# Performance work log

Measured on AMD Instinct MI355X. Metric: run time of the kernel, lower is better.

Reference implementation:

```python
import jax, jax.numpy as jnp
import numpy as np


def _rpad(x):
    # reflect-pad by 1 on both sides along the last dim (matches torch helper)
    return jnp.concatenate([x[..., 1:2], x, x[..., -2:-1]], axis=-1)


def _fwd1d(x):
    # LeGall 5/3 forward lifting along the last dim
    even = x[..., 0::2]
    odd = x[..., 1::2]
    e = _rpad(even)
    pred = 0.5 * (e[..., :-2] + e[..., 2:])
    d = odd - pred                      # detail
    de = _rpad(d)
    upd = 0.25 * (de[..., :-2] + de[..., 2:])
    s = even + upd                      # approx
    return s, d


def setup_inputs() -> dict:
    key = jax.random.key(0)
    # (B, C, H, W) with even H, W so the odd-size reflect pad branch is inactive
    x = jax.random.normal(key, (8, 3, 1024, 1024), dtype=jnp.float32)
    return {"x": x}


def reference(x):
    # rows: transform along W (last dim)
    s_row, d_row = _fwd1d(x)
    # columns: transform along H by swapping H<->W, lifting, swapping back
    LL, LH = _fwd1d(jnp.swapaxes(s_row, 2, 3))
    HL, HH = _fwd1d(jnp.swapaxes(d_row, 2, 3))
    LL, LH, HL, HH = (jnp.swapaxes(t, 2, 3) for t in (LL, LH, HL, HH))
    # (B, 4C, H/2, W/2) subband order [LL, LH, HL, HH]
    return jnp.concatenate([LL, LH, HL, HH], axis=1)
```

## Files before the change

### kernel.cpp

```cpp
#include <hip/hip_runtime.h>


static __device__ __forceinline__ int mref(int k) {
    if (k < 0) return 1;
    if (k > 511) return 510;
    return k;
}

__global__ __launch_bounds__(256) void ilwt53_fused(const float* __restrict__ x,
                                                    float* __restrict__ out) {
    const int tid = threadIdx.x;
    const int c0  = blockIdx.x * 32;
    const int r0  = blockIdx.y * 32;
    const int img = blockIdx.z;

    const int cb = 2 * c0 - 4;
    const int rb = 2 * r0 - 4;

    __shared__ float xt[72 * 73];
    __shared__ float db[72 * 35];
    __shared__ float sb[72 * 33];

    const float* __restrict__ xim = x + (size_t)img * (1024 * 1024);

    #pragma unroll
    for (int n = 0; n < 21; ++n) {
        int i = tid + n * 256;
        if (i < 72 * 72) {
            int lr = i / 72, lc = i - lr * 72;
            int gy = rb + lr; gy = gy < 0 ? 0 : (gy > 1023 ? 1023 : gy);
            int gx = cb + lc; gx = gx < 0 ? 0 : (gx > 1023 ? 1023 : gx);
            xt[lr * 73 + lc] = xim[(size_t)gy * 1024 + gx];
        }
    }
    __syncthreads();

    for (int n = 0; n < 10; ++n) {
        int i = tid + n * 256;
        if (i < 72 * 34) {
            int lr = i / 34, j = i - lr * 34;
            int c = c0 - 1 + j;
            int km1 = mref(c - 1), kp1 = mref(c + 1);
            const float* row = xt + lr * 73;
            float o  = row[2 * (c - c0) + 5];
            float em = row[2 * (km1 - c0) + 4];
            float ep = row[2 * (kp1 - c0) + 4];
            db[lr * 35 + j] = o - 0.5f * (em + ep);
        }
    }
    __syncthreads();

    #pragma unroll
    for (int n = 0; n < 9; ++n) {
        int i = tid + n * 256;
        int lr = i / 32, jj = i & 31;
        int c = c0 + jj;
        int km1 = mref(c - 1), kp1 = mref(c + 1);
        float e  = xt[lr * 73 + 2 * jj + 4];
        float dm = db[lr * 35 + (km1 - c0 + 1)];
        float dp = db[lr * 35 + (kp1 - c0 + 1)];
        sb[lr * 33 + jj] = e + 0.25f * (dm + dp);
    }
    __syncthreads();

    const size_t plane = 512 * 512;
    float* __restrict__ ob = out + ((size_t)(img / 3) * 12 + (img % 3)) * plane;

    #pragma unroll
    for (int p = 0; p < 4; ++p) {
        int i  = tid + p * 256;
        int rr = i >> 5, cc = i & 31;
        int r = r0 + rr, c = c0 + cc;

        const float* sc = sb + cc;
        const float* dc = db + cc + 1;

        auto SE = [&](int k) { return sc[(2 * (k - r0) + 4) * 33]; };
        auto SO = [&](int k) { return sc[(2 * (k - r0) + 5) * 33]; };
        auto DE = [&](int k) { return dc[(2 * (k - r0) + 4) * 35]; };
        auto DO = [&](int k) { return dc[(2 * (k - r0) + 5) * 35]; };

        auto LHf = [&](int k) { return SO(k) - 0.5f * (SE(mref(k - 1)) + SE(mref(k + 1))); };
        auto HHf = [&](int k) { return DO(k) - 0.5f * (DE(mref(k - 1)) + DE(mref(k + 1))); };

        int km = mref(r - 1), kp = mref(r + 1);

        float lh = LHf(r);
        float ll = SE(r) + 0.25f * (LHf(km) + LHf(kp));
        float hh = HHf(r);
        float hl = DE(r) + 0.25f * (HHf(km) + HHf(kp));

        size_t o = (size_t)r * 512 + c;
        ob[o]             = ll;
        ob[o + 3 * plane] = lh;
        ob[o + 6 * plane] = hl;
        ob[o + 9 * plane] = hh;
    }
}

extern "C" void kernel_launch(void* const* d_in, const int* in_sizes, int n_in,
                              void* d_out, int out_size, void* d_ws, size_t ws_size,
                              hipStream_t stream) {
    const float* x = (const float*)d_in[0];
    float* out = (float*)d_out;
    dim3 grid(16, 16, 24);
    dim3 block(256);
    hipLaunchKernelGGL(ilwt53_fused, grid, block, 0, stream, x, out);
}
```

Baseline: 193.3 us.

## Replace shared-memory tiled kernel with register-streaming row-sliding float4 kernel

Replaces the shared-memory tile approach with a kernel where each thread owns four output columns and walks down sixteen output rows. It computes the horizontal lifting from direct float4 global row loads and keeps a sliding window of vertical lifting state in registers. This removes the LDS staging, the three block barriers and the 72x72 halo tile, and it writes outputs as float4. The cost is redundant horizontal recomputation for the halo rows at each 16-row chunk start, more registers per thread, and only 768 blocks of 128 threads.

```diff
diff --git a/kernel.cpp b/kernel.cpp
--- a/kernel.cpp
+++ b/kernel.cpp
@@ -2,99 +2,114 @@
 
 
 static __device__ __forceinline__ int mref(int k) {
-    if (k < 0) return 1;
-    if (k > 511) return 510;
-    return k;
+    return k < 0 ? 1 : (k > 511 ? 510 : k);
 }
 
-__global__ __launch_bounds__(256) void ilwt53_fused(const float* __restrict__ x,
-                                                    float* __restrict__ out) {
-    const int tid = threadIdx.x;
-    const int c0  = blockIdx.x * 32;
-    const int r0  = blockIdx.y * 32;
-    const int img = blockIdx.z;
+static __device__ __forceinline__ float4 f4_sub_half(float4 o, float4 a, float4 b) {
+    return make_float4(o.x - 0.5f * (a.x + b.x), o.y - 0.5f * (a.y + b.y),
+                       o.z - 0.5f * (a.z + b.z), o.w - 0.5f * (a.w + b.w));
+}
+static __device__ __forceinline__ float4 f4_add_q(float4 e, float4 a, float4 b) {
+    return make_float4(e.x + 0.25f * (a.x + b.x), e.y + 0.25f * (a.y + b.y),
+                       e.z + 0.25f * (a.z + b.z), e.w + 0.25f * (a.w + b.w));
+}
 
-    const int cb = 2 * c0 - 4;
-    const int rb = 2 * r0 - 4;
+struct SD { float4 s, d; };
 
-    __shared__ float xt[72 * 73];
-    __shared__ float db[72 * 35];
-    __shared__ float sb[72 * 33];
+static __device__ __forceinline__ SD hrow(const float* __restrict__ xim, int y, int fb) {
+    y = y < 0 ? 0 : (y > 1023 ? 1023 : y);
+    const float* __restrict__ row = xim + (size_t)y * 1024;
+    int fbc = fb < 0 ? 0 : (fb > 1008 ? 1008 : fb);
+
+    float w[16];
+    {
+        const float4* p = (const float4*)(row + fbc);
+        float4 v0 = p[0], v1 = p[1], v2 = p[2], v3 = p[3];
+        w[0]=v0.x; w[1]=v0.y; w[2]=v0.z; w[3]=v0.w;
+        w[4]=v1.x; w[5]=v1.y; w[6]=v1.z; w[7]=v1.w;
+        w[8]=v2.x; w[9]=v2.y; w[10]=v2.z; w[11]=v2.w;
+        w[12]=v3.x; w[13]=v3.y; w[14]=v3.z; w[15]=v3.w;
+    }
+    if (fb < 0) {
+        #pragma unroll
+        for (int q = 15; q >= 4; --q) w[q] = w[q - 4];
+    }
+    if (fb > 1008) {
+        #pragma unroll
+        for (int q = 0; q <= 11; ++q) w[q] = w[q + 4];
+    }
+
+    float d[6];
+    #pragma unroll
+    for (int t = 0; t < 6; ++t)
+        d[t] = w[2*t + 3] - 0.5f * (w[2*t] + w[2*t + 4]);
+    if (fb < 0)    d[1] = w[5]  - w[6];
+    if (fb > 1008) d[4] = w[11] - w[8];
+
+    float4 s;
+    s.x = w[4]  + 0.25f * (d[0] + d[2]);
+    s.y = w[6]  + 0.25f * (d[1] + d[3]);
+    s.z = w[8]  + 0.25f * (d[2] + d[4]);
+    s.w = w[10] + 0.25f * (d[3] + d[5]);
+    if (fb < 0)    s.x = w[4]  + 0.5f * d[2];
+    if (fb > 1008) s.w = w[10] + 0.5f * d[3];
+
+    SD r; r.s = s; r.d = make_float4(d[1], d[2], d[3], d[4]);
+    return r;
+}
+
+__global__ __launch_bounds__(128) void ilwt53_v4(const float* __restrict__ x,
+                                                 float* __restrict__ out) {
+    const int c   = 4 * threadIdx.x;
+    const int fb  = 2 * c - 4;
+    const int R   = 16 * blockIdx.x;
+    const int img = blockIdx.y;
 
     const float* __restrict__ xim = x + (size_t)img * (1024 * 1024);
+    const size_t plane = 512 * 512;
+    float* __restrict__ ob = out + ((size_t)(img / 3) * 12 + (img % 3)) * plane + c;
 
-    #pragma unroll
-    for (int n = 0; n < 21; ++n) {
-        int i = tid + n * 256;
-        if (i < 72 * 72) {
-            int lr = i / 72, lc = i - lr * 72;
-            int gy = rb + lr; gy = gy < 0 ? 0 : (gy > 1023 ? 1023 : gy);
-            int gx = cb + lc; gx = gx < 0 ? 0 : (gx > 1023 ? 1023 : gx);
-            xt[lr * 73 + lc] = xim[(size_t)gy * 1024 + gx];
-        }
+    float4 sEa, dEa, sEb, dEb, sOc, dOc, lhm, hhm, lh0, hh0;
+    {
+        SD a  = hrow(xim, 2 * R, fb);                 sEa = a.s;  dEa = a.d;
+        SD b  = hrow(xim, 2 * (R + 1), fb);           sEb = b.s;  dEb = b.d;
+        SD oc = hrow(xim, 2 * (R + 1) + 1, fb);       sOc = oc.s; dOc = oc.d;
+        SD o0 = hrow(xim, 2 * R + 1, fb);
+        SD em = hrow(xim, 2 * mref(R - 1), fb);
+        lh0 = f4_sub_half(o0.s, em.s, sEb);
+        hh0 = f4_sub_half(o0.d, em.d, dEb);
+        int kA = mref(R - 1);
+        SD oA  = hrow(xim, 2 * kA + 1, fb);
+        SD eAm = hrow(xim, 2 * mref(kA - 1), fb);
+        SD eAp = hrow(xim, 2 * mref(kA + 1), fb);
+        lhm = f4_sub_half(oA.s, eAm.s, eAp.s);
+        hhm = f4_sub_half(oA.d, eAm.d, eAp.d);
     }
-    __syncthreads();
 
-    for (int n = 0; n < 10; ++n) {
-        int i = tid + n * 256;
-        if (i < 72 * 34) {
-            int lr = i / 34, j = i - lr * 34;
-            int c = c0 - 1 + j;
-            int km1 = mref(c - 1), kp1 = mref(c + 1);
-            const float* row = xt + lr * 73;
-            float o  = row[2 * (c - c0) + 5];
-            float em = row[2 * (km1 - c0) + 4];
-            float ep = row[2 * (kp1 - c0) + 4];
-            db[lr * 35 + j] = o - 0.5f * (em + ep);
-        }
-    }
-    __syncthreads();
+    #pragma unroll 8
+    for (int r = R; r < R + 16; ++r) {
+        SD e2 = hrow(xim, 2 * r + 4, fb);
+        SD o2 = hrow(xim, 2 * r + 5, fb);
 
-    #pragma unroll
-    for (int n = 0; n < 9; ++n) {
-        int i = tid + n * 256;
-        int lr = i / 32, jj = i & 31;
-        int c = c0 + jj;
-        int km1 = mref(c - 1), kp1 = mref(c + 1);
-        float e  = xt[lr * 73 + 2 * jj + 4];
-        float dm = db[lr * 35 + (km1 - c0 + 1)];
-        float dp = db[lr * 35 + (kp1 - c0 + 1)];
-        sb[lr * 33 + jj] = e + 0.25f * (dm + dp);
-    }
-    __syncthreads();
+        float4 sE2 = e2.s, dE2 = e2.d;
+        if (r == 510) { sE2 = sEa; dE2 = dEa; }
 
-    const size_t plane = 512 * 512;
-    float* __restrict__ ob = out + ((size_t)(img / 3) * 12 + (img % 3)) * plane;
+        float4 lh1 = f4_sub_half(sOc, sEa, sE2);
+        float4 hh1 = f4_sub_half(dOc, dEa, dE2);
+        if (r == 511) { lh1 = lhm; hh1 = hhm; }
 
-    #pragma unroll
-    for (int p = 0; p < 4; ++p) {
-        int i  = tid + p * 256;
-        int rr = i >> 5, cc = i & 31;
-        int r = r0 + rr, c = c0 + cc;
+        float4 LL = f4_add_q(sEa, lhm, lh1);
+        float4 HL = f4_add_q(dEa, hhm, hh1);
 
-        const float* sc = sb + cc;
-        const float* dc = db + cc + 1;
+        size_t o = (size_t)r * 512;
+        *(float4*)(ob + o)             = LL;
+        *(float4*)(ob + o + 3 * plane) = lh0;
+        *(float4*)(ob + o + 6 * plane) = HL;
+        *(float4*)(ob + o + 9 * plane) = hh0;
 
-        auto SE = [&](int k) { return sc[(2 * (k - r0) + 4) * 33]; };
-        auto SO = [&](int k) { return sc[(2 * (k - r0) + 5) * 33]; };
-        auto DE = [&](int k) { return dc[(2 * (k - r0) + 4) * 35]; };
-        auto DO = [&](int k) { return dc[(2 * (k - r0) + 5) * 35]; };
-
-        auto LHf = [&](int k) { return SO(k) - 0.5f * (SE(mref(k - 1)) + SE(mref(k + 1))); };
-        auto HHf = [&](int k) { return DO(k) - 0.5f * (DE(mref(k - 1)) + DE(mref(k + 1))); };
-
-        int km = mref(r - 1), kp = mref(r + 1);
-
-        float lh = LHf(r);
-        float ll = SE(r) + 0.25f * (LHf(km) + LHf(kp));
-        float hh = HHf(r);
-        float hl = DE(r) + 0.25f * (HHf(km) + HHf(kp));
-
-        size_t o = (size_t)r * 512 + c;
-        ob[o]             = ll;
-        ob[o + 3 * plane] = lh;
-        ob[o + 6 * plane] = hl;
-        ob[o + 9 * plane] = hh;
+        lhm = lh0; lh0 = lh1; hhm = hh0; hh0 = hh1;
+        sEa = sEb; dEa = dEb; sEb = e2.s; dEb = e2.d;
+        sOc = o2.s; dOc = o2.d;
     }
 }
 
@@ -103,7 +118,7 @@
                               hipStream_t stream) {
     const float* x = (const float*)d_in[0];
     float* out = (float*)d_out;
-    dim3 grid(16, 16, 24);
-    dim3 block(256);
-    hipLaunchKernelGGL(ilwt53_fused, grid, block, 0, stream, x, out);
+    dim3 grid(32, 24);
+    dim3 block(128);
+    hipLaunchKernelGGL(ilwt53_v4, grid, block, 0, stream, x, out);
 }
```

Result: faster. 181.6 us (-6.1%).
